# Optimization experiments

Measured on AMD Instinct MI355X. Metric: run time of the kernel, lower is better.

## Reference

```python
import jax, jax.numpy as jnp
import numpy as np

D_MODEL = 1024
NUM_HEADS = 16
D_K = D_MODEL // NUM_HEADS
SCALE = 1.0 / (D_K ** 0.5)


def setup_inputs() -> dict:
    key = jax.random.key(0)
    k1, k2, k3 = jax.random.split(key, 3)
    x = jax.random.normal(k1, (2, 2048, D_MODEL), dtype=jnp.float32)
    # torch nn.Linear weight layout: [out_features, in_features]; y = x @ W.T
    w_qkv = jax.random.normal(k2, (3 * D_MODEL, D_MODEL), dtype=jnp.float32) * (1.0 / np.sqrt(D_MODEL))
    w_out = jax.random.normal(k3, (D_MODEL, D_MODEL), dtype=jnp.float32) * (1.0 / np.sqrt(D_MODEL))
    return {"x": x, "w_qkv": w_qkv, "w_out": w_out}


def reference(x, w_qkv, w_out):
    b, s, _ = x.shape
    qkv = jnp.einsum("bsd,ed->bse", x, w_qkv)            # [b, s, 3*d_model]
    q, k, v = jnp.split(qkv, 3, axis=-1)
    # [b, s, h, d_k] -> [b, h, s, d_k]
    q = q.reshape(b, s, NUM_HEADS, D_K).transpose(0, 2, 1, 3)
    k = k.reshape(b, s, NUM_HEADS, D_K).transpose(0, 2, 1, 3)
    v = v.reshape(b, s, NUM_HEADS, D_K).transpose(0, 2, 1, 3)
    scores = jnp.einsum("bhqd,bhkd->bhqk", q, k) * SCALE   # [b, h, s, s]
    attn = jax.nn.softmax(scores, axis=-1)
    ctx = jnp.einsum("bhqk,bhkd->bhqd", attn, v)           # [b, h, s, d_k]
    ctx = ctx.transpose(0, 2, 1, 3).reshape(b, s, D_MODEL)
    return jnp.einsum("bsd,ed->bse", ctx, w_out)
```

## Files before the change

kernel.cpp:

```cpp
#include <hip/hip_runtime.h>

typedef __attribute__((ext_vector_type(8))) short bf16x8;
typedef __attribute__((ext_vector_type(4))) float f32x4;
typedef __attribute__((ext_vector_type(16))) float f32x16;
typedef __attribute__((ext_vector_type(4))) unsigned int u32x4;

#define MFMA16(A, B, C) __builtin_amdgcn_mfma_f32_16x16x32_bf16((A), (B), (C), 0, 0, 0)
#define MFMA32(A, B, C) __builtin_amdgcn_mfma_f32_32x32x16_bf16((A), (B), (C), 0, 0, 0)

static __device__ __forceinline__ unsigned short f32_to_bf16(float f) {
    unsigned int u = __builtin_bit_cast(unsigned int, f);
    u += 0x7fffu + ((u >> 16) & 1u);
    return (unsigned short)(u >> 16);
}

static __device__ __forceinline__ unsigned int cvtpk(float lo, float hi) {
    unsigned int r;
    asm("v_cvt_pk_bf16_f32 %0, %1, %2" : "=v"(r) : "v"(lo), "v"(hi));
    return r;
}

static __device__ __forceinline__ void gload16(const unsigned short* g, unsigned short* l) {
    __builtin_amdgcn_global_load_lds(
        (const __attribute__((address_space(1))) unsigned int*)g,
        (__attribute__((address_space(3))) unsigned int*)l, 16, 0, 0);
}

#define QSCALE 0.18033688011112042f

__global__ void cast3_f32_bf16(const float* __restrict__ x, const float* __restrict__ wq,
                               const float* __restrict__ wo,
                               unsigned short* __restrict__ xb, unsigned short* __restrict__ wqb,
                               unsigned short* __restrict__ wob) {
    int i = blockIdx.x * 256 + threadIdx.x;
    const float* src;
    unsigned short* dst;
    int off;
    if (i < 1048576)      { src = x;  dst = xb;  off = i; }
    else if (i < 1835008) { src = wq; dst = wqb; off = i - 1048576; }
    else                  { src = wo; dst = wob; off = i - 1835008; }
    float4 v = reinterpret_cast<const float4*>(src)[off];
    ushort4 o;
    o.x = f32_to_bf16(v.x);
    o.y = f32_to_bf16(v.y);
    o.z = f32_to_bf16(v.z);
    o.w = f32_to_bf16(v.w);
    reinterpret_cast<ushort4*>(dst)[off] = o;
}

template <int MODE>
__global__ __launch_bounds__(256, 2)
void gemm_bt(const unsigned short* __restrict__ Ag,
             const unsigned short* __restrict__ Bg,
             int N, int K,
             unsigned short* __restrict__ qO,
             unsigned short* __restrict__ kO,
             unsigned short* __restrict__ vO,
             float* __restrict__ fO)
{
    constexpr int BM = 128, BN = 128, BK = 64;
    __shared__ unsigned short sA[BM * BK];
    __shared__ unsigned short sB[BN * BK];

    const int m0 = blockIdx.y * BM;
    const int n0 = blockIdx.x * BN;
    const int t = threadIdx.x;
    const int lane = t & 63;
    const int wid = t >> 6;
    const int wr = wid >> 1, wc = wid & 1;
    const int g = lane >> 4, r = lane & 15;
    const int lr8 = lane >> 3, lc = lane & 7;

    const f32x4 fzero = {0.f, 0.f, 0.f, 0.f};
    f32x4 acc[4][4];
#pragma unroll
    for (int mi = 0; mi < 4; ++mi)
#pragma unroll
        for (int ni = 0; ni < 4; ++ni) acc[mi][ni] = fzero;

    for (int k0 = 0; k0 < K; k0 += BK) {
        __syncthreads();
#pragma unroll
        for (int rep = 0; rep < 4; ++rep) {
            const int rbase = rep * 32 + wid * 8;
            const int row = rbase + lr8;
            const int cs = lc ^ (row & 7);
            gload16(&Ag[(size_t)(m0 + row) * K + k0 + cs * 8], &sA[rbase * 64]);
            gload16(&Bg[(size_t)(n0 + row) * K + k0 + cs * 8], &sB[rbase * 64]);
        }
        __syncthreads();

#pragma unroll
        for (int ks = 0; ks < BK; ks += 32) {
            const int c = (ks >> 3) + g;
            bf16x8 af[4], bfr[4];
#pragma unroll
            for (int mi = 0; mi < 4; ++mi) {
                const int row = wr * 64 + mi * 16 + r;
                af[mi] = *reinterpret_cast<const bf16x8*>(&sA[row * BK + ((c * 8) ^ ((row & 7) * 8))]);
            }
#pragma unroll
            for (int ni = 0; ni < 4; ++ni) {
                const int row = wc * 64 + ni * 16 + r;
                bfr[ni] = *reinterpret_cast<const bf16x8*>(&sB[row * BK + ((c * 8) ^ ((row & 7) * 8))]);
            }
#pragma unroll
            for (int mi = 0; mi < 4; ++mi)
#pragma unroll
                for (int ni = 0; ni < 4; ++ni)
                    acc[mi][ni] = MFMA16(af[mi], bfr[ni], acc[mi][ni]);
        }
    }

#pragma unroll
    for (int mi = 0; mi < 4; ++mi) {
#pragma unroll
        for (int ni = 0; ni < 4; ++ni) {
            const int mbase = m0 + wr * 64 + mi * 16 + 4 * g;
            const int n = n0 + wc * 64 + ni * 16 + r;
            if (MODE == 0) {
                const int b = mbase >> 11, s = mbase & 2047;
                const int which = n >> 10;
                const int h = (n >> 6) & 15;
                const int d = n & 63;
                if (which == 2) {
                    ushort4 v4;
                    v4.x = f32_to_bf16(acc[mi][ni][0]);
                    v4.y = f32_to_bf16(acc[mi][ni][1]);
                    v4.z = f32_to_bf16(acc[mi][ni][2]);
                    v4.w = f32_to_bf16(acc[mi][ni][3]);
                    *reinterpret_cast<ushort4*>(&vO[(((size_t)(b * 16 + h)) * 64 + d) * 2048 + s]) = v4;
                } else {
                    const size_t dst = (((size_t)(b * 16 + h)) * 2048 + s) * 64 + d;
#pragma unroll
                    for (int i = 0; i < 4; ++i) {
                        const float val = acc[mi][ni][i];
                        if (which == 0) qO[dst + (size_t)i * 64] = f32_to_bf16(val * QSCALE);
                        else            kO[dst + (size_t)i * 64] = f32_to_bf16(val);
                    }
                }
            } else {
#pragma unroll
                for (int i = 0; i < 4; ++i)
                    fO[(size_t)(mbase + i) * N + n] = acc[mi][ni][i];
            }
        }
    }
}

__global__ __launch_bounds__(512, 4)
void attn_kernel(const unsigned short* __restrict__ Q,
                 const unsigned short* __restrict__ Kg,
                 const unsigned short* __restrict__ Vtg,
                 unsigned short* __restrict__ ctx)
{
    const int S = 2048;
    const int bid = blockIdx.x;
    const int swz = (bid & 7) * 64 + (bid >> 3);
    const int hb = swz >> 4;
    const int qb = swz & 15;
    const unsigned short* Qh = Q + (size_t)hb * S * 64;
    const unsigned short* Kh = Kg + (size_t)hb * S * 64;
    const unsigned short* Vh = Vtg + (size_t)hb * 64 * S;

    const int t = threadIdx.x, lane = t & 63, wid = t >> 6;
    const int half = wid >> 2, wq = wid & 3;
    const int l31 = lane & 31, lhi = lane >> 5;
    const int lr8 = lane >> 3, lc = lane & 7;
    const int q0 = qb * 128 + wq * 32;
    const int kbase = half * 1024;

    const int krow = (l31 & 19) | ((l31 & 4) << 1) | ((l31 & 8) >> 1);
    const int ksw = (krow & 7) ^ ((krow >> 3) & 3);
    const int vsw = (l31 & 7) ^ ((l31 >> 3) & 3);

    __shared__ unsigned short smem[2][2][2][64 * 64];

    bf16x8 qf[4];
#pragma unroll
    for (int dstep = 0; dstep < 4; ++dstep)
        qf[dstep] = *reinterpret_cast<const bf16x8*>(
            &Qh[(size_t)(q0 + l31) * 64 + dstep * 16 + lhi * 8]);

    f32x16 acc[2];
#pragma unroll
    for (int dt = 0; dt < 2; ++dt)
#pragma unroll
        for (int i = 0; i < 16; ++i) acc[dt][i] = 0.f;
    float lrun = 0.f;

#define STAGE(buf, k0)                                                                       \
    {                                                                                        \
        _Pragma("unroll")                                                                    \
        for (int rep = 0; rep < 2; ++rep) {                                                  \
            const int rbase = wq * 16 + rep * 8;                                             \
            const int row = rbase + lr8;                                                     \
            const int cs = lc ^ ((row & 7) ^ ((row >> 3) & 3));                              \
            gload16(&Kh[(size_t)((k0) + row) * 64 + cs * 8], &smem[half][buf][0][rbase * 64]); \
            gload16(&Vh[(size_t)row * S + (k0) + cs * 8], &smem[half][buf][1][rbase * 64]);  \
        }                                                                                    \
    }

    STAGE(0, kbase);

    for (int it = 0; it < 16; ++it) {
        __syncthreads();
        const int cur = it & 1;
        if (it < 15) {
            const int kn = kbase + (it + 1) * 64;
            if (cur) STAGE(0, kn) else STAGE(1, kn);
        }
        const unsigned short* kb = smem[half][cur][0];
        const unsigned short* vb = smem[half][cur][1];

        f32x16 st0, st1;
#pragma unroll
        for (int i = 0; i < 16; ++i) { st0[i] = 0.f; st1[i] = 0.f; }
        __builtin_amdgcn_s_setprio(1);
#pragma unroll
        for (int dstep = 0; dstep < 4; ++dstep) {
            const int c = dstep * 2 + lhi;
            bf16x8 kf0 = *reinterpret_cast<const bf16x8*>(&kb[krow * 64 + ((c ^ ksw) * 8)]);
            bf16x8 kf1 = *reinterpret_cast<const bf16x8*>(&kb[(32 + krow) * 64 + ((c ^ ksw) * 8)]);
            st0 = MFMA32(kf0, qf[dstep], st0);
            st1 = MFMA32(kf1, qf[dstep], st1);
        }
        __builtin_amdgcn_s_setprio(0);

#pragma unroll
        for (int i = 0; i < 16; ++i) {
            st0[i] = __builtin_amdgcn_exp2f(st0[i]);
            st1[i] = __builtin_amdgcn_exp2f(st1[i]);
        }
        float s8[8];
#pragma unroll
        for (int j = 0; j < 8; ++j)
            s8[j] = (st0[j] + st0[j + 8]) + (st1[j] + st1[j + 8]);
        lrun += ((s8[0] + s8[1]) + (s8[2] + s8[3])) + ((s8[4] + s8[5]) + (s8[6] + s8[7]));

        bf16x8 pf[4];
#define PACK8(stv, base, out)                                                  \
        {                                                                      \
            u32x4 wv;                                                          \
            wv[0] = cvtpk(stv[(base) + 0], stv[(base) + 1]);                   \
            wv[1] = cvtpk(stv[(base) + 2], stv[(base) + 3]);                   \
            wv[2] = cvtpk(stv[(base) + 4], stv[(base) + 5]);                   \
            wv[3] = cvtpk(stv[(base) + 6], stv[(base) + 7]);                   \
            out = __builtin_bit_cast(bf16x8, wv);                              \
        }
        PACK8(st0, 0, pf[0])
        PACK8(st0, 8, pf[1])
        PACK8(st1, 0, pf[2])
        PACK8(st1, 8, pf[3])
#undef PACK8

        __builtin_amdgcn_s_setprio(1);
#pragma unroll
        for (int dt = 0; dt < 2; ++dt) {
            const int rowd = dt * 32 + l31;
#pragma unroll
            for (int ks = 0; ks < 4; ++ks) {
                const int c = ks * 2 + lhi;
                bf16x8 vf = *reinterpret_cast<const bf16x8*>(&vb[rowd * 64 + ((c ^ vsw) * 8)]);
                acc[dt] = MFMA32(vf, pf[ks], acc[dt]);
            }
        }
        __builtin_amdgcn_s_setprio(0);
    }
#undef STAGE

    lrun += __shfl_xor(lrun, 32);

    __syncthreads();
    float* cb = reinterpret_cast<float*>(&smem[0][0][0][0]);
    if (half == 1) {
        float* base = cb + wq * 2112;
#pragma unroll
        for (int dt = 0; dt < 2; ++dt)
#pragma unroll
            for (int i = 0; i < 16; ++i)
                base[(dt * 16 + i) * 64 + lane] = acc[dt][i];
        if (lhi == 0) base[2048 + l31] = lrun;
    }
    __syncthreads();
    if (half == 0) {
        float* base = cb + wq * 2112;
        const float l1 = base[2048 + l31];
        const float rl = __builtin_amdgcn_rcpf(lrun + l1);
        const int b = hb >> 4, hh = hb & 15;
        const size_t rowbase = ((size_t)(b * 2048 + q0 + l31)) * 1024 + hh * 64;
#pragma unroll
        for (int dt = 0; dt < 2; ++dt) {
#pragma unroll
            for (int rg = 0; rg < 4; ++rg) {
                float v0 = (acc[dt][4 * rg + 0] + base[(dt * 16 + 4 * rg + 0) * 64 + lane]) * rl;
                float v1 = (acc[dt][4 * rg + 1] + base[(dt * 16 + 4 * rg + 1) * 64 + lane]) * rl;
                float v2 = (acc[dt][4 * rg + 2] + base[(dt * 16 + 4 * rg + 2) * 64 + lane]) * rl;
                float v3 = (acc[dt][4 * rg + 3] + base[(dt * 16 + 4 * rg + 3) * 64 + lane]) * rl;
                uint2 o;
                o.x = cvtpk(v0, v1);
                o.y = cvtpk(v2, v3);
                const int dbase = dt * 32 + rg * 8 + lhi * 4;
                *reinterpret_cast<uint2*>(&ctx[rowbase + dbase]) = o;
            }
        }
    }
}

extern "C" void kernel_launch(void* const* d_in, const int* in_sizes, int n_in,
                              void* d_out, int out_size, void* d_ws, size_t ws_size,
                              hipStream_t stream) {
    const float* x     = (const float*)d_in[0];
    const float* w_qkv = (const float*)d_in[1];
    const float* w_out = (const float*)d_in[2];
    float* out = (float*)d_out;

    unsigned short* xb    = (unsigned short*)d_ws;
    unsigned short* wqkvb = xb + 4194304;
    unsigned short* woutb = wqkvb + 3145728;
    unsigned short* qB    = woutb + 1048576;
    unsigned short* kB    = qB + 4194304;
    unsigned short* vB    = kB + 4194304;
    unsigned short* ctxB  = vB + 4194304;

    cast3_f32_bf16<<<8192, 256, 0, stream>>>(x, w_qkv, w_out, xb, wqkvb, woutb);

    gemm_bt<0><<<dim3(24, 32), 256, 0, stream>>>(xb, wqkvb, 3072, 1024, qB, kB, vB, nullptr);

    attn_kernel<<<512, 512, 0, stream>>>(qB, kB, vB, ctxB);

    gemm_bt<1><<<dim3(8, 32), 256, 0, stream>>>(ctxB, woutb, 1024, 1024, nullptr, nullptr, nullptr, out);
}
```

Before: 106.8 us.

## Software-pipeline QK^T one tile ahead with triple-buffered K and split V staging

Result: slower. 324.1 us (+203.6%).

```diff
diff --git a/kernel.cpp b/kernel.cpp
--- a/kernel.cpp
+++ b/kernel.cpp
@@ -174,7 +174,8 @@
     const int ksw = (krow & 7) ^ ((krow >> 3) & 3);
     const int vsw = (l31 & 7) ^ ((l31 >> 3) & 3);
 
-    __shared__ unsigned short smem[2][2][2][64 * 64];
+    __shared__ unsigned short sK[2][3][64 * 64];
+    __shared__ unsigned short sV[2][2][64 * 64];
 
     bf16x8 qf[4];
 #pragma unroll
@@ -189,53 +190,71 @@
         for (int i = 0; i < 16; ++i) acc[dt][i] = 0.f;
     float lrun = 0.f;
 
-#define STAGE(buf, k0)                                                                       \
-    {                                                                                        \
-        _Pragma("unroll")                                                                    \
-        for (int rep = 0; rep < 2; ++rep) {                                                  \
-            const int rbase = wq * 16 + rep * 8;                                             \
-            const int row = rbase + lr8;                                                     \
-            const int cs = lc ^ ((row & 7) ^ ((row >> 3) & 3));                              \
-            gload16(&Kh[(size_t)((k0) + row) * 64 + cs * 8], &smem[half][buf][0][rbase * 64]); \
-            gload16(&Vh[(size_t)row * S + (k0) + cs * 8], &smem[half][buf][1][rbase * 64]);  \
-        }                                                                                    \
-    }
-
-    STAGE(0, kbase);
-
-    for (int it = 0; it < 16; ++it) {
-        __syncthreads();
-        const int cur = it & 1;
-        if (it < 15) {
-            const int kn = kbase + (it + 1) * 64;
-            if (cur) STAGE(0, kn) else STAGE(1, kn);
-        }
-        const unsigned short* kb = smem[half][cur][0];
-        const unsigned short* vb = smem[half][cur][1];
-
-        f32x16 st0, st1;
-#pragma unroll
-        for (int i = 0; i < 16; ++i) { st0[i] = 0.f; st1[i] = 0.f; }
+#define STAGE_K(buf, k0)                                                                   \
+    {                                                                                      \
+        _Pragma("unroll")                                                                  \
+        for (int rep = 0; rep < 2; ++rep) {                                                \
+            const int rbase = wq * 16 + rep * 8;                                           \
+            const int row = rbase + lr8;                                                   \
+            const int cs = lc ^ ((row & 7) ^ ((row >> 3) & 3));                            \
+            gload16(&Kh[(size_t)((k0) + row) * 64 + cs * 8], &sK[half][buf][rbase * 64]);  \
+        }                                                                                  \
+    }
+#define STAGE_V(buf, k0)                                                                   \
+    {                                                                                      \
+        _Pragma("unroll")                                                                  \
+        for (int rep = 0; rep < 2; ++rep) {                                                \
+            const int rbase = wq * 16 + rep * 8;                                           \
+            const int row = rbase + lr8;                                                   \
+            const int cs = lc ^ ((row & 7) ^ ((row >> 3) & 3));                            \
+            gload16(&Vh[(size_t)row * S + (k0) + cs * 8], &sV[half][buf][rbase * 64]);     \
+        }                                                                                  \
+    }
+
+    auto QKSTEP = [&](int kslot, f32x16& o0, f32x16& o1) {
+#pragma unroll
+        for (int i = 0; i < 16; ++i) { o0[i] = 0.f; o1[i] = 0.f; }
+        const unsigned short* kb = &sK[half][kslot][0];
         __builtin_amdgcn_s_setprio(1);
 #pragma unroll
         for (int dstep = 0; dstep < 4; ++dstep) {
             const int c = dstep * 2 + lhi;
             bf16x8 kf0 = *reinterpret_cast<const bf16x8*>(&kb[krow * 64 + ((c ^ ksw) * 8)]);
             bf16x8 kf1 = *reinterpret_cast<const bf16x8*>(&kb[(32 + krow) * 64 + ((c ^ ksw) * 8)]);
-            st0 = MFMA32(kf0, qf[dstep], st0);
-            st1 = MFMA32(kf1, qf[dstep], st1);
+            o0 = MFMA32(kf0, qf[dstep], o0);
+            o1 = MFMA32(kf1, qf[dstep], o1);
         }
         __builtin_amdgcn_s_setprio(0);
+    };
+
+    int kc = 0, kn = 1, ks2 = 2;
+    int vc = 0;
+
+    STAGE_K(0, kbase);
+    STAGE_K(1, kbase + 64);
+    asm volatile("s_waitcnt vmcnt(2)" ::: "memory");
+    __builtin_amdgcn_s_barrier();
+    STAGE_V(0, kbase);
+    f32x16 stA0, stA1, stB0, stB1;
+    QKSTEP(0, stA0, stA1);
+
+    auto BODY = [&](int it, f32x16& in0, f32x16& in1, f32x16& out0, f32x16& out1) {
+        if (it < 14) STAGE_K(ks2, kbase + (it + 2) * 64);
+        if (it < 14) asm volatile("s_waitcnt vmcnt(2)" ::: "memory");
+        else         asm volatile("s_waitcnt vmcnt(0)" ::: "memory");
+        __builtin_amdgcn_s_barrier();
+        if (it < 15) STAGE_V(vc ^ 1, kbase + (it + 1) * 64);
+        if (it < 15) QKSTEP(kn, out0, out1);
 
 #pragma unroll
         for (int i = 0; i < 16; ++i) {
-            st0[i] = __builtin_amdgcn_exp2f(st0[i]);
-            st1[i] = __builtin_amdgcn_exp2f(st1[i]);
+            in0[i] = __builtin_amdgcn_exp2f(in0[i]);
+            in1[i] = __builtin_amdgcn_exp2f(in1[i]);
         }
         float s8[8];
 #pragma unroll
         for (int j = 0; j < 8; ++j)
-            s8[j] = (st0[j] + st0[j + 8]) + (st1[j] + st1[j + 8]);
+            s8[j] = (in0[j] + in0[j + 8]) + (in1[j] + in1[j + 8]);
         lrun += ((s8[0] + s8[1]) + (s8[2] + s8[3])) + ((s8[4] + s8[5]) + (s8[6] + s8[7]));
 
         bf16x8 pf[4];
@@ -248,31 +267,41 @@
             wv[3] = cvtpk(stv[(base) + 6], stv[(base) + 7]);                   \
             out = __builtin_bit_cast(bf16x8, wv);                              \
         }
-        PACK8(st0, 0, pf[0])
-        PACK8(st0, 8, pf[1])
-        PACK8(st1, 0, pf[2])
-        PACK8(st1, 8, pf[3])
+        PACK8(in0, 0, pf[0])
+        PACK8(in0, 8, pf[1])
+        PACK8(in1, 0, pf[2])
+        PACK8(in1, 8, pf[3])
 #undef PACK8
 
+        const unsigned short* vb = &sV[half][vc][0];
         __builtin_amdgcn_s_setprio(1);
 #pragma unroll
         for (int dt = 0; dt < 2; ++dt) {
             const int rowd = dt * 32 + l31;
 #pragma unroll
-            for (int ks = 0; ks < 4; ++ks) {
-                const int c = ks * 2 + lhi;
+            for (int ksl = 0; ksl < 4; ++ksl) {
+                const int c = ksl * 2 + lhi;
                 bf16x8 vf = *reinterpret_cast<const bf16x8*>(&vb[rowd * 64 + ((c ^ vsw) * 8)]);
-                acc[dt] = MFMA32(vf, pf[ks], acc[dt]);
+                acc[dt] = MFMA32(vf, pf[ksl], acc[dt]);
             }
         }
         __builtin_amdgcn_s_setprio(0);
-    }
-#undef STAGE
+
+        const int tmp = kc; kc = kn; kn = ks2; ks2 = tmp;
+        vc ^= 1;
+    };
+
+    for (int t2 = 0; t2 < 16; t2 += 2) {
+        BODY(t2,     stA0, stA1, stB0, stB1);
+        BODY(t2 + 1, stB0, stB1, stA0, stA1);
+    }
+#undef STAGE_K
+#undef STAGE_V
 
     lrun += __shfl_xor(lrun, 32);
 
     __syncthreads();
-    float* cb = reinterpret_cast<float*>(&smem[0][0][0][0]);
+    float* cb = reinterpret_cast<float*>(&sK[0][0][0]);
     if (half == 1) {
         float* base = cb + wq * 2112;
 #pragma unroll
```
